# Performance work log

Hardware: AMD Instinct MI355X
Metric: run time of the kernel (lower is better)

Reference implementation:

```python
import jax, jax.numpy as jnp
import numpy as np

D_MODEL = 1024
NUM_HEADS = 16
D_K = D_MODEL // NUM_HEADS
D_FF = 4096
EPS = 1e-6


def setup_inputs() -> dict:
    key = jax.random.key(0)
    ks = jax.random.split(key, 12)
    B, S = 4, 1024
    s = 1.0 / np.sqrt(D_MODEL)
    return {
        "x": jax.random.normal(ks[0], (B, S, D_MODEL), dtype=jnp.float32),
        "ln1_g": jnp.ones((D_MODEL,), jnp.float32),
        "ln1_b": jnp.zeros((D_MODEL,), jnp.float32),
        "wq": jax.random.normal(ks[1], (D_MODEL, D_MODEL), jnp.float32) * s,
        "wk": jax.random.normal(ks[2], (D_MODEL, D_MODEL), jnp.float32) * s,
        "wv": jax.random.normal(ks[3], (D_MODEL, D_MODEL), jnp.float32) * s,
        "wo": jax.random.normal(ks[4], (D_MODEL, D_MODEL), jnp.float32) * s,
        "ln2_g": jnp.ones((D_MODEL,), jnp.float32),
        "ln2_b": jnp.zeros((D_MODEL,), jnp.float32),
        "w1": jax.random.normal(ks[5], (D_MODEL, D_FF), jnp.float32) * s,
        "b1": jnp.zeros((D_FF,), jnp.float32),
        "w2": jax.random.normal(ks[6], (D_FF, D_MODEL), jnp.float32) * (1.0 / np.sqrt(D_FF)),
        "b2": jnp.zeros((D_MODEL,), jnp.float32),
    }


def _layernorm(x, g, b):
    mu = jnp.mean(x, axis=-1, keepdims=True)
    var = jnp.var(x, axis=-1, keepdims=True)
    return (x - mu) * jax.lax.rsqrt(var + EPS) * g + b


def _mha(x, wq, wk, wv, wo):
    B, S, _ = x.shape
    # project and split heads: [B,S,D] -> [B,H,S,Dk]
    q = (x @ wq).reshape(B, S, NUM_HEADS, D_K).transpose(0, 2, 1, 3)
    k = (x @ wk).reshape(B, S, NUM_HEADS, D_K).transpose(0, 2, 1, 3)
    v = (x @ wv).reshape(B, S, NUM_HEADS, D_K).transpose(0, 2, 1, 3)
    scores = jnp.einsum("bhqd,bhkd->bhqk", q, k) / np.sqrt(D_K).astype(np.float32)
    attn = jax.nn.softmax(scores, axis=-1)  # no mask: source forwards mask=None
    out = jnp.einsum("bhqk,bhkd->bhqd", attn, v)
    out = out.transpose(0, 2, 1, 3).reshape(B, S, D_MODEL)
    return out @ wo


def reference(x, ln1_g, ln1_b, wq, wk, wv, wo, ln2_g, ln2_b, w1, b1, w2, b2):
    x1 = _layernorm(x, ln1_g, ln1_b)
    x = x + _mha(x1, wq, wk, wv, wo)  # dropout identity (eval)
    x2 = _layernorm(x, ln2_g, ln2_b)
    ffn = jax.nn.relu(x2 @ w1 + b1) @ w2 + b2
    return x + ffn
```

## Files before the change

kernel.cpp:

```cpp
#include <hip/hip_runtime.h>

typedef __bf16 bf16;
typedef __bf16 bf16x8 __attribute__((ext_vector_type(8)));
typedef __bf16 bf16x4 __attribute__((ext_vector_type(4)));
typedef float f32x4 __attribute__((ext_vector_type(4)));

__device__ __forceinline__ void gload_lds16(const void* g, void* l) {
  __builtin_amdgcn_global_load_lds(
      (const __attribute__((address_space(1))) unsigned int*)g,
      (__attribute__((address_space(3))) unsigned int*)l, 16, 0, 0);
}

__global__ __launch_bounds__(256) void transpose_cast(const float* __restrict__ src,
                                                      bf16* __restrict__ dst,
                                                      int R, int C) {
  __shared__ float tile[32][33];
  const int tx = threadIdx.x & 31, ty = threadIdx.x >> 5;
  const int c0 = blockIdx.x * 32, r0 = blockIdx.y * 32;
#pragma unroll
  for (int i = 0; i < 4; i++)
    tile[ty + i * 8][tx] = src[(size_t)(r0 + ty + i * 8) * C + c0 + tx];
  __syncthreads();
#pragma unroll
  for (int i = 0; i < 4; i++)
    dst[(size_t)(c0 + ty + i * 8) * R + r0 + tx] = (bf16)tile[tx][ty + i * 8];
}

__global__ __launch_bounds__(256) void ln_kernel(const float* __restrict__ x,
                                                 const float* __restrict__ g,
                                                 const float* __restrict__ b,
                                                 bf16* __restrict__ y) {
  const int w = threadIdx.x >> 6, lane = threadIdx.x & 63;
  const int row = blockIdx.x * 4 + w;
  const float* xr = x + (size_t)row * 1024;
  float4 v[4];
  float s = 0.f, sq = 0.f;
#pragma unroll
  for (int c = 0; c < 4; c++) {
    v[c] = *reinterpret_cast<const float4*>(xr + c * 256 + lane * 4);
    s += v[c].x + v[c].y + v[c].z + v[c].w;
    sq += v[c].x * v[c].x + v[c].y * v[c].y + v[c].z * v[c].z + v[c].w * v[c].w;
  }
#pragma unroll
  for (int d = 32; d >= 1; d >>= 1) {
    s += __shfl_xor(s, d, 64);
    sq += __shfl_xor(sq, d, 64);
  }
  const float mu = s * (1.f / 1024.f);
  const float rs = rsqrtf(sq * (1.f / 1024.f) - mu * mu + 1e-6f);
#pragma unroll
  for (int c = 0; c < 4; c++) {
    float4 gv = *reinterpret_cast<const float4*>(g + c * 256 + lane * 4);
    float4 bv = *reinterpret_cast<const float4*>(b + c * 256 + lane * 4);
    bf16x4 ov;
    ov[0] = (bf16)((v[c].x - mu) * rs * gv.x + bv.x);
    ov[1] = (bf16)((v[c].y - mu) * rs * gv.y + bv.y);
    ov[2] = (bf16)((v[c].z - mu) * rs * gv.z + bv.z);
    ov[3] = (bf16)((v[c].w - mu) * rs * gv.w + bv.w);
    *reinterpret_cast<bf16x4*>(y + (size_t)row * 1024 + c * 256 + lane * 4) = ov;
  }
}

__global__ __launch_bounds__(256) void reduce_ln_kernel(const bf16* __restrict__ p0,
                                                        const bf16* __restrict__ p1,
                                                        const float* __restrict__ x,
                                                        const float* __restrict__ g,
                                                        const float* __restrict__ b,
                                                        float* __restrict__ xres,
                                                        bf16* __restrict__ y) {
  const int w = threadIdx.x >> 6, lane = threadIdx.x & 63;
  const int row = blockIdx.x * 4 + w;
  const size_t rb = (size_t)row * 1024;
  float4 v[4];
  float s = 0.f, sq = 0.f;
#pragma unroll
  for (int c = 0; c < 4; c++) {
    const int off = c * 256 + lane * 4;
    float4 xv = *reinterpret_cast<const float4*>(x + rb + off);
    bf16x4 a0 = *reinterpret_cast<const bf16x4*>(p0 + rb + off);
    bf16x4 a1 = *reinterpret_cast<const bf16x4*>(p1 + rb + off);
    v[c].x = xv.x + (float)a0[0] + (float)a1[0];
    v[c].y = xv.y + (float)a0[1] + (float)a1[1];
    v[c].z = xv.z + (float)a0[2] + (float)a1[2];
    v[c].w = xv.w + (float)a0[3] + (float)a1[3];
    *reinterpret_cast<float4*>(xres + rb + off) = v[c];
    s += v[c].x + v[c].y + v[c].z + v[c].w;
    sq += v[c].x * v[c].x + v[c].y * v[c].y + v[c].z * v[c].z + v[c].w * v[c].w;
  }
#pragma unroll
  for (int d = 32; d >= 1; d >>= 1) {
    s += __shfl_xor(s, d, 64);
    sq += __shfl_xor(sq, d, 64);
  }
  const float mu = s * (1.f / 1024.f);
  const float rs = rsqrtf(sq * (1.f / 1024.f) - mu * mu + 1e-6f);
#pragma unroll
  for (int c = 0; c < 4; c++) {
    const int off = c * 256 + lane * 4;
    float4 gv = *reinterpret_cast<const float4*>(g + off);
    float4 bv = *reinterpret_cast<const float4*>(b + off);
    bf16x4 ov;
    ov[0] = (bf16)((v[c].x - mu) * rs * gv.x + bv.x);
    ov[1] = (bf16)((v[c].y - mu) * rs * gv.y + bv.y);
    ov[2] = (bf16)((v[c].z - mu) * rs * gv.z + bv.z);
    ov[3] = (bf16)((v[c].w - mu) * rs * gv.w + bv.w);
    *reinterpret_cast<bf16x4*>(y + rb + off) = ov;
  }
}

__global__ __launch_bounds__(256) void reduce_out_kernel(const bf16* __restrict__ p0,
                                                         const bf16* __restrict__ p1,
                                                         const bf16* __restrict__ p2,
                                                         const bf16* __restrict__ p3,
                                                         const float* __restrict__ bias,
                                                         const float* __restrict__ xres,
                                                         float* __restrict__ out) {
  const size_t i = ((size_t)blockIdx.x * 256 + threadIdx.x) * 8;
  const int col = (int)(i & 1023);
  bf16x8 a0 = *reinterpret_cast<const bf16x8*>(p0 + i);
  bf16x8 a1 = *reinterpret_cast<const bf16x8*>(p1 + i);
  bf16x8 a2 = *reinterpret_cast<const bf16x8*>(p2 + i);
  bf16x8 a3 = *reinterpret_cast<const bf16x8*>(p3 + i);
  float4 r0 = *reinterpret_cast<const float4*>(xres + i);
  float4 r1 = *reinterpret_cast<const float4*>(xres + i + 4);
  float4 b0 = *reinterpret_cast<const float4*>(bias + col);
  float4 b1 = *reinterpret_cast<const float4*>(bias + col + 4);
  float4 o0, o1;
  o0.x = r0.x + b0.x + (float)a0[0] + (float)a1[0] + (float)a2[0] + (float)a3[0];
  o0.y = r0.y + b0.y + (float)a0[1] + (float)a1[1] + (float)a2[1] + (float)a3[1];
  o0.z = r0.z + b0.z + (float)a0[2] + (float)a1[2] + (float)a2[2] + (float)a3[2];
  o0.w = r0.w + b0.w + (float)a0[3] + (float)a1[3] + (float)a2[3] + (float)a3[3];
  o1.x = r1.x + b1.x + (float)a0[4] + (float)a1[4] + (float)a2[4] + (float)a3[4];
  o1.y = r1.y + b1.y + (float)a0[5] + (float)a1[5] + (float)a2[5] + (float)a3[5];
  o1.z = r1.z + b1.z + (float)a0[6] + (float)a1[6] + (float)a2[6] + (float)a3[6];
  o1.w = r1.w + b1.w + (float)a0[7] + (float)a1[7] + (float)a2[7] + (float)a3[7];
  *reinterpret_cast<float4*>(out + i) = o0;
  *reinterpret_cast<float4*>(out + i + 4) = o1;
}

template <int EPI>
__global__ __launch_bounds__(256) void gemm_bt(const bf16* __restrict__ A,
                                               const bf16* __restrict__ Bt,
                                               void* __restrict__ Cout,
                                               const float* __restrict__ bias,
                                               int M, int N, int K, int gy, int gxy,
                                               int Kc) {
  __shared__ __align__(16) bf16 As[2][128][32];
  __shared__ __align__(16) bf16 Bs[2][128][32];
  const int tid = threadIdx.x;
  const int w = tid >> 6, lane = tid & 63;
  const int wr = w >> 1, wc = w & 1;

  const int nwg = gridDim.x;
  const int cpx = nwg >> 3;
  const int swz = (blockIdx.x & 7) * cpx + (blockIdx.x >> 3);
  const int chunk = swz / gxy, rem = swz % gxy;
  const int gpc = gy << 3;
  const int band = rem / gpc, r2 = rem % gpc;
  const int bm = (band * 8 + (r2 & 7)) * 128;
  const int bn = (r2 >> 3) * 128;

  f32x4 acc[4][4] = {};
  const int r4 = lane >> 2;
  const int c8 = (lane & 3) * 8;
  const bf16* Ag = A + (size_t)(bm + w * 32 + r4) * K + chunk * Kc + c8;
  const bf16* Bg = Bt + (size_t)(bn + w * 32 + r4) * K + chunk * Kc + c8;
  const int fr = lane & 15, fo = (lane >> 4) * 8;

#define STAGE(buf, k0)                                                 \
  do {                                                                 \
    gload_lds16(Ag + (k0), &As[buf][w * 32][0]);                       \
    gload_lds16(Ag + (size_t)16 * K + (k0), &As[buf][w * 32 + 16][0]); \
    gload_lds16(Bg + (k0), &Bs[buf][w * 32][0]);                       \
    gload_lds16(Bg + (size_t)16 * K + (k0), &Bs[buf][w * 32 + 16][0]); \
  } while (0)

  const int nt = Kc >> 5;
  STAGE(0, 0);
  __syncthreads();
  int cur = 0;
  for (int t = 0; t < nt; ++t) {
    if (t + 1 < nt) STAGE(cur ^ 1, (t + 1) << 5);
    bf16x8 af[4], bfr[4];
#pragma unroll
    for (int m = 0; m < 4; m++)
      af[m] = *reinterpret_cast<const bf16x8*>(&As[cur][wr * 64 + m * 16 + fr][fo]);
#pragma unroll
    for (int n = 0; n < 4; n++)
      bfr[n] = *reinterpret_cast<const bf16x8*>(&Bs[cur][wc * 64 + n * 16 + fr][fo]);
#pragma unroll
    for (int m = 0; m < 4; m++)
#pragma unroll
      for (int n = 0; n < 4; n++)
        acc[m][n] = __builtin_amdgcn_mfma_f32_16x16x32_bf16(af[m], bfr[n], acc[m][n], 0, 0, 0);
    __syncthreads();
    cur ^= 1;
  }
#undef STAGE

  bf16* outp = (bf16*)Cout + (EPI == 3 ? (size_t)chunk * M * N : 0);
  const int cr = (lane >> 4) * 4, cc = lane & 15;
#pragma unroll
  for (int m = 0; m < 4; m++) {
#pragma unroll
    for (int n = 0; n < 4; n++) {
      const int row = bm + wr * 64 + m * 16 + cr;
      const int col = bn + wc * 64 + n * 16 + cc;
#pragma unroll
      for (int r = 0; r < 4; r++) {
        const float va = acc[m][n][r];
        const size_t idx = (size_t)(row + r) * N + col;
        if (EPI == 0 || EPI == 3) {
          outp[idx] = (bf16)va;
        } else {
          const float t = va + bias[col];
          outp[idx] = (bf16)(t > 0.f ? t : 0.f);
        }
      }
    }
  }
}

template <int EPI>
__global__ __launch_bounds__(512, 2) void gemm256(const bf16* __restrict__ A,
                                                  const bf16* __restrict__ Bt,
                                                  void* __restrict__ Cout,
                                                  const float* __restrict__ bias,
                                                  int M, int N, int K, int gy, int gxy,
                                                  int Kc) {
  __shared__ __align__(16) bf16 As[2][256][64];
  __shared__ __align__(16) bf16 Bs[2][256][64];
  const int tid = threadIdx.x;
  const int w = tid >> 6, lane = tid & 63;
  const int wm = w >> 2, wn = w & 3;
  const int fr = lane & 15, g = lane >> 4;

  const int nwg = gridDim.x;
  const int cpx = nwg >> 3;
  const int swz = (blockIdx.x & 7) * cpx + (blockIdx.x >> 3);
  const int chunk = swz / gxy, rem = swz % gxy;
  const int gpc = gy << 3;
  const int band = rem / gpc, r2 = rem % gpc;
  const int bm = (band * 8 + (r2 & 7)) * 256;
  const int bn = (r2 >> 3) * 256;

  const bf16* Ab = A + (size_t)bm * K;
  const bf16* Bb = Bt + (size_t)bn * K;

  const int lr = lane >> 3;
  const int sle = ((lane & 7) ^ lr) * 8;
  const int rB0 = w * 16;
  const int rB1 = 128 + w * 16;
  const int rA0 = wm * 128 + wn * 16;
  const int rA1 = wm * 128 + 64 + wn * 16;

  char* AsB = (char*)&As[0][0][0];
  char* BsB = (char*)&Bs[0][0][0];
  const int rowA = (wm * 128 + fr) * 128;
  const int rowB = (wn * 64 + fr) * 128;
  const int colk0 = (g * 16) ^ ((fr & 7) << 4);
  const int colk1 = (64 + g * 16) ^ ((fr & 7) << 4);

  f32x4 acc[8][4] = {};

#define SG8(base, r0, kb, ldsrow)                                           \
  do {                                                                      \
    gload_lds16(base + (size_t)((r0) + lr) * K + (kb) + sle, (ldsrow));     \
    gload_lds16(base + (size_t)((r0) + 8 + lr) * K + (kb) + sle,            \
                (char*)(ldsrow) + 1024);                                    \
  } while (0)

  const int nt = Kc >> 6;
  const int koff = chunk * Kc;

  SG8(Bb, rB0, koff, BsB + rB0 * 128);
  SG8(Bb, rB1, koff, BsB + rB1 * 128);
  SG8(Ab, rA0, koff, AsB + rA0 * 128);
  SG8(Ab, rA1, koff, AsB + rA1 * 128);

#define PHASE_BODY(p, mb)                                                     \
  {                                                                           \
    if ((p) == 0) {                                                           \
      _Pragma("unroll") for (int nf = 0; nf < 4; nf++) {                      \
        bfr[nf][0] = *(const bf16x8*)(Br + rowB + nf * 2048 + colk0);         \
        bfr[nf][1] = *(const bf16x8*)(Br + rowB + nf * 2048 + colk1);         \
      }                                                                       \
    }                                                                         \
    af[0][0] = *(const bf16x8*)(Ar + rowA + (mb)*2048 + colk0);               \
    af[0][1] = *(const bf16x8*)(Ar + rowA + (mb)*2048 + colk1);               \
    af[1][0] = *(const bf16x8*)(Ar + rowA + ((mb) + 1) * 2048 + colk0);       \
    af[1][1] = *(const bf16x8*)(Ar + rowA + ((mb) + 1) * 2048 + colk1);       \
    if (pre) {                                                                \
      if ((p) == 0) SG8(Bb, rB0, kb2, Bw + rB0 * 128);                        \
      if ((p) == 1) SG8(Bb, rB1, kb2, Bw + rB1 * 128);                        \
      if ((p) == 2) SG8(Ab, rA0, kb2, Aw + rA0 * 128);                        \
      if ((p) == 3) SG8(Ab, rA1, kb2, Aw + rA1 * 128);                        \
    }                                                                         \
    __builtin_amdgcn_s_setprio(1);                                            \
    _Pragma("unroll") for (int m2 = 0; m2 < 2; m2++)                          \
        _Pragma("unroll") for (int nf = 0; nf < 4; nf++) {                    \
      acc[(mb) + m2][nf] = __builtin_amdgcn_mfma_f32_16x16x32_bf16(           \
          af[m2][0], bfr[nf][0], acc[(mb) + m2][nf], 0, 0, 0);                \
      acc[(mb) + m2][nf] = __builtin_amdgcn_mfma_f32_16x16x32_bf16(           \
          af[m2][1], bfr[nf][1], acc[(mb) + m2][nf], 0, 0, 0);                \
    }                                                                         \
    __builtin_amdgcn_s_setprio(0);                                            \
  }

  int buf = 0;
  for (int kt = 0; kt < nt; ++kt) {
    char* Ar = AsB + buf * 32768;
    char* Br = BsB + buf * 32768;
    char* Aw = AsB + (buf ^ 1) * 32768;
    char* Bw = BsB + (buf ^ 1) * 32768;
    const bool pre = (kt + 1) < nt;
    const int kb2 = koff + (kt + 1) * 64;
    bf16x8 bfr[4][2];
    bf16x8 af[2][2];

    asm volatile("s_waitcnt vmcnt(2)" ::: "memory");
    __builtin_amdgcn_s_barrier();
    PHASE_BODY(0, 0)

    if (pre) asm volatile("s_waitcnt vmcnt(4)" ::: "memory");
    else     asm volatile("s_waitcnt vmcnt(2)" ::: "memory");
    __builtin_amdgcn_s_barrier();
    PHASE_BODY(1, 2)

    if (pre) asm volatile("s_waitcnt vmcnt(4)" ::: "memory");
    else     asm volatile("s_waitcnt vmcnt(0)" ::: "memory");
    __builtin_amdgcn_s_barrier();
    PHASE_BODY(2, 4)

    if (pre) asm volatile("s_waitcnt vmcnt(6)" ::: "memory");
    else     asm volatile("s_waitcnt vmcnt(0)" ::: "memory");
    __builtin_amdgcn_s_barrier();
    PHASE_BODY(3, 6)

    buf ^= 1;
  }
#undef PHASE_BODY
#undef SG8

  bf16* outp = (bf16*)Cout + (EPI == 3 ? (size_t)chunk * M * N : 0);
  const int cr = g * 4;
#pragma unroll
  for (int mf = 0; mf < 8; mf++) {
#pragma unroll
    for (int nf = 0; nf < 4; nf++) {
      const int row = bm + wm * 128 + mf * 16 + cr;
      const int col = bn + wn * 64 + nf * 16 + fr;
#pragma unroll
      for (int r = 0; r < 4; r++) {
        const float va = acc[mf][nf][r];
        const size_t idx = (size_t)(row + r) * N + col;
        if (EPI == 3 || EPI == 0) {
          outp[idx] = (bf16)va;
        } else {
          const float t = va + bias[col];
          outp[idx] = (bf16)(t > 0.f ? t : 0.f);
        }
      }
    }
  }
}

__global__ __launch_bounds__(512, 4) void attn_kernel(const bf16* __restrict__ Q,
                                                      const bf16* __restrict__ K,
                                                      const bf16* __restrict__ V,
                                                      bf16* __restrict__ O, int ld) {
  __shared__ __align__(16) bf16 Ks[2][64][64];
  __shared__ __align__(16) bf16 Vt[2][64][64];
  __shared__ __align__(16) bf16 Pl[8][16][64];
  const int tid = threadIdx.x;
  const int w = tid >> 6, l = tid & 63;
  const int lo = l & 15, g = l >> 4;
  const int sw = (lo & 7) << 3;

  const int id = blockIdx.x;
  const int bh = id & 63, qb = id >> 6;
  const int b = bh >> 4, h = bh & 15;
  const int hoff = h * 64;
  const size_t rowQ = (size_t)b * 1024 + qb * 128 + w * 16;
  const size_t rowKV0 = (size_t)b * 1024;

  const int srow = tid >> 3, scch = tid & 7;
  const int vcb = w * 8;

  bf16x8 qfr[2];
#pragma unroll
  for (int ds = 0; ds < 2; ds++)
    qfr[ds] = *reinterpret_cast<const bf16x8*>(
        Q + (rowQ + lo) * ld + hoff + ds * 32 + g * 8);

  const float c = 0.18033688f;
  f32x4 lacc = {0.f, 0.f, 0.f, 0.f};
  f32x4 o[4] = {};

  {
    gload_lds16(K + (rowKV0 + srow) * ld + hoff + ((scch ^ (srow & 7)) << 3),
                &Ks[0][w * 8][0]);
    bf16x8 vv = *reinterpret_cast<const bf16x8*>(V + (rowKV0 + l) * ld + hoff + vcb);
#pragma unroll
    for (int j = 0; j < 8; j++) Vt[0][vcb + j][l ^ (j << 3)] = vv[j];
  }
  __syncthreads();

#define ATILE(PAR, KT)                                                               \
  {                                                                                  \
    bf16x8 vv;                                                                       \
    const bool more = (KT) + 1 < 16;                                                 \
    if (more) {                                                                      \
      const size_t rkv = rowKV0 + ((KT) + 1) * 64;                                   \
      gload_lds16(K + (rkv + srow) * ld + hoff + ((scch ^ (srow & 7)) << 3),         \
                  &Ks[(PAR) ^ 1][w * 8][0]);                                         \
      vv = *reinterpret_cast<const bf16x8*>(V + (rkv + l) * ld + hoff + vcb);        \
    }                                                                                \
    f32x4 sa[4] = {};                                                                \
    _Pragma("unroll") for (int ds = 0; ds < 2; ds++) {                               \
      bf16x8 kf[4];                                                                  \
      _Pragma("unroll") for (int kfi = 0; kfi < 4; kfi++)                            \
          kf[kfi] = *reinterpret_cast<const bf16x8*>(                                \
              &Ks[PAR][kfi * 16 + lo][(ds * 32 + g * 8) ^ sw]);                      \
      _Pragma("unroll") for (int kfi = 0; kfi < 4; kfi++)                            \
          sa[kfi] =                                                                  \
              __builtin_amdgcn_mfma_f32_16x16x32_bf16(kf[kfi], qfr[ds], sa[kfi], 0, 0, 0); \
    }                                                                                \
    float p[16];                                                                     \
    _Pragma("unroll") for (int kfi = 0; kfi < 4; kfi++)                              \
        _Pragma("unroll") for (int r = 0; r < 4; r++)                                \
            p[kfi * 4 + r] = exp2f(sa[kfi][r] * c);                                  \
    _Pragma("unroll") for (int r = 0; r < 4; r++)                                    \
        lacc[r] += (p[r] + p[4 + r]) + (p[8 + r] + p[12 + r]);                       \
    _Pragma("unroll") for (int kfi = 0; kfi < 4; kfi++) {                            \
      bf16x4 pk;                                                                     \
      pk[0] = (bf16)p[kfi * 4 + 0];                                                  \
      pk[1] = (bf16)p[kfi * 4 + 1];                                                  \
      pk[2] = (bf16)p[kfi * 4 + 2];                                                  \
      pk[3] = (bf16)p[kfi * 4 + 3];                                                  \
      *reinterpret_cast<bf16x4*>(&Pl[w][lo][(kfi * 16 + g * 4) ^ sw]) = pk;          \
    }                                                                                \
    _Pragma("unroll") for (int ks = 0; ks < 2; ks++) {                               \
      bf16x8 pf = *reinterpret_cast<const bf16x8*>(&Pl[w][lo][(ks * 32 + g * 8) ^ sw]); \
      _Pragma("unroll") for (int df = 0; df < 4; df++) {                             \
        bf16x8 vf = *reinterpret_cast<const bf16x8*>(                                \
            &Vt[PAR][df * 16 + lo][(ks * 32 + g * 8) ^ sw]);                         \
        o[df] = __builtin_amdgcn_mfma_f32_16x16x32_bf16(vf, pf, o[df], 0, 0, 0);     \
      }                                                                              \
    }                                                                                \
    if (more) {                                                                      \
      _Pragma("unroll") for (int j = 0; j < 8; j++)                                  \
          Vt[(PAR) ^ 1][vcb + j][l ^ (j << 3)] = vv[j];                              \
    }                                                                                \
    __syncthreads();                                                                 \
  }

  for (int kt2 = 0; kt2 < 16; kt2 += 2) {
    ATILE(0, kt2)
    ATILE(1, kt2 + 1)
  }
#undef ATILE

  float lsum = (lacc[0] + lacc[1]) + (lacc[2] + lacc[3]);
  lsum += __shfl_xor(lsum, 16);
  lsum += __shfl_xor(lsum, 32);
  const float rl = 1.f / lsum;
#pragma unroll
  for (int df = 0; df < 4; df++) {
    bf16x4 ov;
#pragma unroll
    for (int r = 0; r < 4; r++) ov[r] = (bf16)(o[df][r] * rl);
    *reinterpret_cast<bf16x4*>(&Pl[w][lo][(df * 16 + g * 4) ^ sw]) = ov;
  }
  const int row = l >> 2;
  const int swr = (row & 7) << 3;
  const int c2 = (l & 3) * 16;
#pragma unroll
  for (int i = 0; i < 2; i++) {
    bf16x8 ov = *reinterpret_cast<const bf16x8*>(&Pl[w][row][(c2 + i * 8) ^ swr]);
    *reinterpret_cast<bf16x8*>(O + (rowQ + row) * 1024 + hoff + c2 + i * 8) = ov;
  }
}

extern "C" void kernel_launch(void* const* d_in, const int* in_sizes, int n_in,
                              void* d_out, int out_size, void* d_ws, size_t ws_size,
                              hipStream_t stream) {
  const float* x     = (const float*)d_in[0];
  const float* ln1_g = (const float*)d_in[1];
  const float* ln1_b = (const float*)d_in[2];
  const float* wq    = (const float*)d_in[3];
  const float* wk    = (const float*)d_in[4];
  const float* wv    = (const float*)d_in[5];
  const float* wo    = (const float*)d_in[6];
  const float* ln2_g = (const float*)d_in[7];
  const float* ln2_b = (const float*)d_in[8];
  const float* w1    = (const float*)d_in[9];
  const float* b1    = (const float*)d_in[10];
  const float* w2    = (const float*)d_in[11];
  const float* b2    = (const float*)d_in[12];

  const size_t MB = 1ull << 20;
  char* ws = (char*)d_ws;
  bf16* wTqkv = (bf16*)(ws + 0 * MB);
  bf16* wTo   = (bf16*)(ws + 6 * MB);
  bf16* wT1   = (bf16*)(ws + 8 * MB);
  bf16* wT2   = (bf16*)(ws + 16 * MB);
  bf16* x1    = (bf16*)(ws + 24 * MB);
  bf16* qkv   = (bf16*)(ws + 32 * MB);
  float* xres = (float*)(ws + 56 * MB);
  bf16* h1    = (bf16*)(ws + 72 * MB);
  bf16* attn  = x1;
  bf16* x2    = qkv;
  bf16* pOp   = (bf16*)(ws + 40 * MB);
  bf16* pF    = (bf16*)(ws + 24 * MB);

  const dim3 TB(256);

  transpose_cast<<<dim3(32, 32), TB, 0, stream>>>(wq, wTqkv, 1024, 1024);
  transpose_cast<<<dim3(32, 32), TB, 0, stream>>>(wk, wTqkv + 1024 * 1024, 1024, 1024);
  transpose_cast<<<dim3(32, 32), TB, 0, stream>>>(wv, wTqkv + 2048 * 1024, 1024, 1024);
  transpose_cast<<<dim3(32, 32), TB, 0, stream>>>(wo, wTo, 1024, 1024);
  transpose_cast<<<dim3(128, 32), TB, 0, stream>>>(w1, wT1, 1024, 4096);
  transpose_cast<<<dim3(32, 128), TB, 0, stream>>>(w2, wT2, 4096, 1024);

  ln_kernel<<<1024, TB, 0, stream>>>(x, ln1_g, ln1_b, x1);

  gemm256<0><<<192, dim3(512), 0, stream>>>(x1, wTqkv, qkv, nullptr, 4096, 3072, 1024, 12, 192, 1024);

  attn_kernel<<<512, dim3(512), 0, stream>>>(qkv, qkv + 1024, qkv + 2048, attn, 3072);

  gemm_bt<3><<<512, TB, 0, stream>>>(attn, wTo, pOp, nullptr, 4096, 1024, 1024, 8, 256, 512);

  reduce_ln_kernel<<<1024, TB, 0, stream>>>(pOp, pOp + 4096 * 1024, x, ln2_g, ln2_b, xres, x2);

  gemm256<2><<<256, dim3(512), 0, stream>>>(x2, wT1, h1, b1, 4096, 4096, 1024, 16, 256, 1024);

  gemm256<3><<<256, dim3(512), 0, stream>>>(h1, wT2, pF, nullptr, 4096, 1024, 4096, 4, 64, 1024);

  reduce_out_kernel<<<2048, TB, 0, stream>>>(pF, pF + 4096 * 1024, pF + 2 * 4096 * 1024,
                                             pF + 3 * 4096 * 1024, b2, xres, (float*)d_out);
}
```

Measured before the change: 210.0 us.

## Double query rows per attention wave and batch four weight transposes

Each attention wave now handles 32 query rows instead of 16, so each K/V tile loaded into LDS is reused across twice as many queries. The grid is halved to 256 blocks with a remapped block index. Launch bounds drop to 2 blocks per SM and the P buffer grows. Separately, the four 1024x1024 weight transpose-casts are merged into one launch using blockIdx.z. This cuts K/V traffic and launch count, but raises register pressure and lowers occupancy, and 256 blocks may underfill the GPU.

```diff
diff --git a/kernel.cpp b/kernel.cpp
--- a/kernel.cpp
+++ b/kernel.cpp
@@ -24,6 +24,29 @@
 #pragma unroll
   for (int i = 0; i < 4; i++)
     dst[(size_t)(c0 + ty + i * 8) * R + r0 + tx] = (bf16)tile[tx][ty + i * 8];
+}
+
+__global__ __launch_bounds__(256) void transpose_cast4(const float* __restrict__ s0,
+                                                       const float* __restrict__ s1,
+                                                       const float* __restrict__ s2,
+                                                       const float* __restrict__ s3,
+                                                       bf16* __restrict__ d0,
+                                                       bf16* __restrict__ d1,
+                                                       bf16* __restrict__ d2,
+                                                       bf16* __restrict__ d3) {
+  const int z = blockIdx.z;
+  const float* src = z == 0 ? s0 : z == 1 ? s1 : z == 2 ? s2 : s3;
+  bf16* dst = z == 0 ? d0 : z == 1 ? d1 : z == 2 ? d2 : d3;
+  __shared__ float tile[32][33];
+  const int tx = threadIdx.x & 31, ty = threadIdx.x >> 5;
+  const int c0 = blockIdx.x * 32, r0 = blockIdx.y * 32;
+#pragma unroll
+  for (int i = 0; i < 4; i++)
+    tile[ty + i * 8][tx] = src[(size_t)(r0 + ty + i * 8) * 1024 + c0 + tx];
+  __syncthreads();
+#pragma unroll
+  for (int i = 0; i < 4; i++)
+    dst[(size_t)(c0 + ty + i * 8) * 1024 + r0 + tx] = (bf16)tile[tx][ty + i * 8];
 }
 
 __global__ __launch_bounds__(256) void ln_kernel(const float* __restrict__ x,
@@ -365,37 +388,40 @@
   }
 }
 
-__global__ __launch_bounds__(512, 4) void attn_kernel(const bf16* __restrict__ Q,
+__global__ __launch_bounds__(512, 2) void attn_kernel(const bf16* __restrict__ Q,
                                                       const bf16* __restrict__ K,
                                                       const bf16* __restrict__ V,
                                                       bf16* __restrict__ O, int ld) {
   __shared__ __align__(16) bf16 Ks[2][64][64];
   __shared__ __align__(16) bf16 Vt[2][64][64];
-  __shared__ __align__(16) bf16 Pl[8][16][64];
+  __shared__ __align__(16) bf16 Pl[8][32][64];
   const int tid = threadIdx.x;
   const int w = tid >> 6, l = tid & 63;
   const int lo = l & 15, g = l >> 4;
   const int sw = (lo & 7) << 3;
 
   const int id = blockIdx.x;
-  const int bh = id & 63, qb = id >> 6;
+  const int bh = (id & 7) | ((id >> 5) << 3);
+  const int qb = (id >> 3) & 3;
   const int b = bh >> 4, h = bh & 15;
   const int hoff = h * 64;
-  const size_t rowQ = (size_t)b * 1024 + qb * 128 + w * 16;
+  const size_t rowQ = (size_t)b * 1024 + qb * 256 + w * 32;
   const size_t rowKV0 = (size_t)b * 1024;
 
   const int srow = tid >> 3, scch = tid & 7;
   const int vcb = w * 8;
 
-  bf16x8 qfr[2];
-#pragma unroll
-  for (int ds = 0; ds < 2; ds++)
-    qfr[ds] = *reinterpret_cast<const bf16x8*>(
-        Q + (rowQ + lo) * ld + hoff + ds * 32 + g * 8);
+  bf16x8 qfr[2][2];
+#pragma unroll
+  for (int qi = 0; qi < 2; qi++)
+#pragma unroll
+    for (int ds = 0; ds < 2; ds++)
+      qfr[qi][ds] = *reinterpret_cast<const bf16x8*>(
+          Q + (rowQ + qi * 16 + lo) * ld + hoff + ds * 32 + g * 8);
 
   const float c = 0.18033688f;
-  f32x4 lacc = {0.f, 0.f, 0.f, 0.f};
-  f32x4 o[4] = {};
+  f32x4 lacc[2] = {};
+  f32x4 o[4][2] = {};
 
   {
     gload_lds16(K + (rowKV0 + srow) * ld + hoff + ((scch ^ (srow & 7)) << 3),
@@ -416,37 +442,45 @@
                   &Ks[(PAR) ^ 1][w * 8][0]);                                         \
       vv = *reinterpret_cast<const bf16x8*>(V + (rkv + l) * ld + hoff + vcb);        \
     }                                                                                \
-    f32x4 sa[4] = {};                                                                \
+    f32x4 sa[4][2] = {};                                                             \
     _Pragma("unroll") for (int ds = 0; ds < 2; ds++) {                               \
       bf16x8 kf[4];                                                                  \
       _Pragma("unroll") for (int kfi = 0; kfi < 4; kfi++)                            \
           kf[kfi] = *reinterpret_cast<const bf16x8*>(                                \
               &Ks[PAR][kfi * 16 + lo][(ds * 32 + g * 8) ^ sw]);                      \
       _Pragma("unroll") for (int kfi = 0; kfi < 4; kfi++)                            \
-          sa[kfi] =                                                                  \
-              __builtin_amdgcn_mfma_f32_16x16x32_bf16(kf[kfi], qfr[ds], sa[kfi], 0, 0, 0); \
+          _Pragma("unroll") for (int qi = 0; qi < 2; qi++)                           \
+              sa[kfi][qi] = __builtin_amdgcn_mfma_f32_16x16x32_bf16(                 \
+                  kf[kfi], qfr[qi][ds], sa[kfi][qi], 0, 0, 0);                       \
     }                                                                                \
-    float p[16];                                                                     \
-    _Pragma("unroll") for (int kfi = 0; kfi < 4; kfi++)                              \
-        _Pragma("unroll") for (int r = 0; r < 4; r++)                                \
-            p[kfi * 4 + r] = exp2f(sa[kfi][r] * c);                                  \
-    _Pragma("unroll") for (int r = 0; r < 4; r++)                                    \
-        lacc[r] += (p[r] + p[4 + r]) + (p[8 + r] + p[12 + r]);                       \
-    _Pragma("unroll") for (int kfi = 0; kfi < 4; kfi++) {                            \
-      bf16x4 pk;                                                                     \
-      pk[0] = (bf16)p[kfi * 4 + 0];                                                  \
-      pk[1] = (bf16)p[kfi * 4 + 1];                                                  \
-      pk[2] = (bf16)p[kfi * 4 + 2];                                                  \
-      pk[3] = (bf16)p[kfi * 4 + 3];                                                  \
-      *reinterpret_cast<bf16x4*>(&Pl[w][lo][(kfi * 16 + g * 4) ^ sw]) = pk;          \
+    _Pragma("unroll") for (int qi = 0; qi < 2; qi++) {                               \
+      float p[16];                                                                   \
+      _Pragma("unroll") for (int kfi = 0; kfi < 4; kfi++)                            \
+          _Pragma("unroll") for (int r = 0; r < 4; r++)                              \
+              p[kfi * 4 + r] = exp2f(sa[kfi][qi][r] * c);                            \
+      _Pragma("unroll") for (int r = 0; r < 4; r++)                                  \
+          lacc[qi][r] += (p[r] + p[4 + r]) + (p[8 + r] + p[12 + r]);                 \
+      _Pragma("unroll") for (int kfi = 0; kfi < 4; kfi++) {                          \
+        bf16x4 pk;                                                                   \
+        pk[0] = (bf16)p[kfi * 4 + 0];                                                \
+        pk[1] = (bf16)p[kfi * 4 + 1];                                                \
+        pk[2] = (bf16)p[kfi * 4 + 2];                                                \
+        pk[3] = (bf16)p[kfi * 4 + 3];                                                \
+        *reinterpret_cast<bf16x4*>(&Pl[w][qi * 16 + lo][(kfi * 16 + g * 4) ^ sw]) = pk; \
+      }                                                                              \
     }                                                                                \
     _Pragma("unroll") for (int ks = 0; ks < 2; ks++) {                               \
-      bf16x8 pf = *reinterpret_cast<const bf16x8*>(&Pl[w][lo][(ks * 32 + g * 8) ^ sw]); \
-      _Pragma("unroll") for (int df = 0; df < 4; df++) {                             \
-        bf16x8 vf = *reinterpret_cast<const bf16x8*>(                                \
-            &Vt[PAR][df * 16 + lo][(ks * 32 + g * 8) ^ sw]);                         \
-        o[df] = __builtin_amdgcn_mfma_f32_16x16x32_bf16(vf, pf, o[df], 0, 0, 0);     \
-      }                                                                              \
+      bf16x8 pf[2], vf[4];                                                           \
+      _Pragma("unroll") for (int qi = 0; qi < 2; qi++)                               \
+          pf[qi] = *reinterpret_cast<const bf16x8*>(                                 \
+              &Pl[w][qi * 16 + lo][(ks * 32 + g * 8) ^ sw]);                         \
+      _Pragma("unroll") for (int df = 0; df < 4; df++)                               \
+          vf[df] = *reinterpret_cast<const bf16x8*>(                                 \
+              &Vt[PAR][df * 16 + lo][(ks * 32 + g * 8) ^ sw]);                       \
+      _Pragma("unroll") for (int df = 0; df < 4; df++)                               \
+          _Pragma("unroll") for (int qi = 0; qi < 2; qi++)                           \
+              o[df][qi] = __builtin_amdgcn_mfma_f32_16x16x32_bf16(                   \
+                  vf[df], pf[qi], o[df][qi], 0, 0, 0);                               \
     }                                                                                \
     if (more) {                                                                      \
       _Pragma("unroll") for (int j = 0; j < 8; j++)                                  \
@@ -461,24 +495,27 @@
   }
 #undef ATILE
 
-  float lsum = (lacc[0] + lacc[1]) + (lacc[2] + lacc[3]);
-  lsum += __shfl_xor(lsum, 16);
-  lsum += __shfl_xor(lsum, 32);
-  const float rl = 1.f / lsum;
-#pragma unroll
-  for (int df = 0; df < 4; df++) {
-    bf16x4 ov;
-#pragma unroll
-    for (int r = 0; r < 4; r++) ov[r] = (bf16)(o[df][r] * rl);
-    *reinterpret_cast<bf16x4*>(&Pl[w][lo][(df * 16 + g * 4) ^ sw]) = ov;
-  }
-  const int row = l >> 2;
+#pragma unroll
+  for (int qi = 0; qi < 2; qi++) {
+    float lsum = (lacc[qi][0] + lacc[qi][1]) + (lacc[qi][2] + lacc[qi][3]);
+    lsum += __shfl_xor(lsum, 16);
+    lsum += __shfl_xor(lsum, 32);
+    const float rl = 1.f / lsum;
+#pragma unroll
+    for (int df = 0; df < 4; df++) {
+      bf16x4 ov;
+#pragma unroll
+      for (int r = 0; r < 4; r++) ov[r] = (bf16)(o[df][qi][r] * rl);
+      *reinterpret_cast<bf16x4*>(&Pl[w][qi * 16 + lo][(df * 16 + g * 4) ^ sw]) = ov;
+    }
+  }
+  const int row = l >> 1;
   const int swr = (row & 7) << 3;
-  const int c2 = (l & 3) * 16;
-#pragma unroll
-  for (int i = 0; i < 2; i++) {
-    bf16x8 ov = *reinterpret_cast<const bf16x8*>(&Pl[w][row][(c2 + i * 8) ^ swr]);
-    *reinterpret_cast<bf16x8*>(O + (rowQ + row) * 1024 + hoff + c2 + i * 8) = ov;
+#pragma unroll
+  for (int i = 0; i < 4; i++) {
+    const int c2 = (l & 1) * 4 + i;
+    bf16x8 ov = *reinterpret_cast<const bf16x8*>(&Pl[w][row][(c2 * 8) ^ swr]);
+    *reinterpret_cast<bf16x8*>(O + (rowQ + row) * 1024 + hoff + c2 * 8) = ov;
   }
 }
 
@@ -516,10 +553,8 @@
 
   const dim3 TB(256);
 
-  transpose_cast<<<dim3(32, 32), TB, 0, stream>>>(wq, wTqkv, 1024, 1024);
-  transpose_cast<<<dim3(32, 32), TB, 0, stream>>>(wk, wTqkv + 1024 * 1024, 1024, 1024);
-  transpose_cast<<<dim3(32, 32), TB, 0, stream>>>(wv, wTqkv + 2048 * 1024, 1024, 1024);
-  transpose_cast<<<dim3(32, 32), TB, 0, stream>>>(wo, wTo, 1024, 1024);
+  transpose_cast4<<<dim3(32, 32, 4), TB, 0, stream>>>(
+      wq, wk, wv, wo, wTqkv, wTqkv + 1024 * 1024, wTqkv + 2048 * 1024, wTo);
   transpose_cast<<<dim3(128, 32), TB, 0, stream>>>(w1, wT1, 1024, 4096);
   transpose_cast<<<dim3(32, 128), TB, 0, stream>>>(w2, wT2, 4096, 1024);
 
@@ -527,7 +562,7 @@
 
   gemm256<0><<<192, dim3(512), 0, stream>>>(x1, wTqkv, qkv, nullptr, 4096, 3072, 1024, 12, 192, 1024);
 
-  attn_kernel<<<512, dim3(512), 0, stream>>>(qkv, qkv + 1024, qkv + 2048, attn, 3072);
+  attn_kernel<<<256, dim3(512), 0, stream>>>(qkv, qkv + 1024, qkv + 2048, attn, 3072);
 
   gemm_bt<3><<<512, TB, 0, stream>>>(attn, wTo, pOp, nullptr, 4096, 1024, 1024, 8, 256, 512);
 
```

Result: no change. 208.1 us (-0.9%).
